# Performance work log

Hardware: AMD Instinct MI355X
Metric: run time of the kernel (lower is better)

Reference implementation:

```python
import jax, jax.numpy as jnp
import numpy as np

N = 4096
IN, HID, OUT = 512, 512, 512
EMB, MHID = 64, 128
GRID_SIZE, SPLINE_ORDER = 5, 3
D_B = GRID_SIZE + SPLINE_ORDER + 1      # 9
SPLINE_DIM = GRID_SIZE + SPLINE_ORDER   # 8


def make_grid():
    h = (1.0 - (-1.0)) / GRID_SIZE
    return jnp.arange(-SPLINE_ORDER, GRID_SIZE + SPLINE_ORDER + 1, dtype=jnp.float32) * h - 1.0


def b_splines(x, grid):
    # x: (N, in) -> (N, in, SPLINE_DIM); Cox-de Boor recursion, epsilon-stabilized
    xg = x[..., None]
    bases = ((xg >= grid[:-1]) & (xg < grid[1:])).astype(x.dtype)
    eps = 1e-08
    for k in range(1, SPLINE_ORDER + 1):
        dp = grid[k:-1] - grid[:-(k + 1)]
        dn = grid[k + 1:] - grid[1:-k]
        bases = (xg - grid[:-(k + 1)]) / (dp + eps) * bases[..., :-1] \
              + (grid[k + 1:] - xg) / (dn + eps) * bases[..., 1:]
    return bases


def _xavier(k, shape):
    fan_out, fan_in = shape
    std = (2.0 / (fan_in + fan_out)) ** 0.5
    return std * jax.random.normal(k, shape, jnp.float32)


def setup_inputs() -> dict:
    key = jax.random.key(0)
    ks = jax.random.split(key, 7)
    x = 2.0 * jax.random.uniform(ks[0], (N, IN), jnp.float32) - 1.0
    inp = {"x": x}
    dims = [(IN, HID), (HID, OUT)]
    for i, (fi, fo) in enumerate(dims):
        kk = jax.random.split(ks[i + 1], 3)
        inp[f"emb{i}"] = _xavier(kk[0], (fi * fo, EMB))   # layout: (out, in) flattened, out outer
        inp[f"w1_{i}"] = _xavier(kk[1], (MHID, EMB))
        inp[f"b1_{i}"] = jnp.zeros((MHID,), jnp.float32)
        inp[f"w2_{i}"] = _xavier(kk[2], (D_B, MHID))
        inp[f"b2_{i}"] = jnp.zeros((D_B,), jnp.float32)
    return inp


def _kan_layer(h, emb, w1, b1, w2, b2, in_f, out_f, grid):
    basis = b_splines(h, grid)                              # (N, in, SPLINE_DIM)
    w = (emb @ w1.T + b1) @ w2.T + b2                       # (out*in, D_B)
    w = w.reshape(out_f, in_f, D_B)
    w_spline = w[..., :SPLINE_DIM]                          # (out, in, SPLINE_DIM)
    w_base = w[..., SPLINE_DIM]                             # (out, in)  == weights[:, :, -1]
    out = jnp.einsum('nis,ois->no', basis, w_spline)
    out = out + jnp.einsum('ni,oi->no', jax.nn.silu(h), w_base)
    return out


def reference(x, emb0, w1_0, b1_0, w2_0, b2_0, emb1, w1_1, b1_1, w2_1, b2_1):
    grid = make_grid()
    h = _kan_layer(x, emb0, w1_0, b1_0, w2_0, b2_0, IN, HID, grid)
    h = _kan_layer(h, emb1, w1_1, b1_1, w2_1, b2_1, HID, OUT, grid)
    return h
```

## Files before the change

### kernel.cpp

```cpp
#include <hip/hip_runtime.h>
#include <cstdint>
#include <cstddef>

typedef unsigned short u16;
typedef unsigned int   u32;

typedef __bf16 bf16x8 __attribute__((ext_vector_type(8)));
typedef float  f32x4  __attribute__((ext_vector_type(4)));

#define NROWS 4096
#define INF   512
#define OUTF  512
#define EMB   64
#define MHID  128
#define DB    9
#define KDIM  (INF * DB)
#define MN    (NROWS * OUTF)

__device__ __forceinline__ u16 f2bf(float f) {
    union { float f; u32 ui; } v; v.f = f;
    u32 u = v.ui;
    u += 0x7fffu + ((u >> 16) & 1u);
    return (u16)(u >> 16);
}
__device__ __forceinline__ float gridv(int t) { return (float)(t - 3) * 0.4f - 1.0f; }

__global__ __launch_bounds__(256) void meff_kernel(
    const float* __restrict__ w1_0, const float* __restrict__ b1_0,
    const float* __restrict__ w2_0, const float* __restrict__ b2_0,
    const float* __restrict__ w1_1, const float* __restrict__ b1_1,
    const float* __restrict__ w2_1, const float* __restrict__ b2_1,
    float* __restrict__ Mc)
{
    int tid  = threadIdx.x;
    int lane = tid & 63;
    int wid  = blockIdx.x * 4 + (tid >> 6);
    if (wid >= 1170) return;
    int layer = wid / 585;
    int o     = wid % 585;
    const float* w1 = layer ? w1_1 : w1_0;
    const float* b1 = layer ? b1_1 : b1_0;
    const float* w2 = layer ? w2_1 : w2_0;
    const float* b2 = layer ? b2_1 : b2_0;

    float p;
    int d;
    if (o < 576) {
        int j = o / 9; d = o % 9;
        p = w1[lane * EMB + j]        * w2[d * MHID + lane]
          + w1[(lane + 64) * EMB + j] * w2[d * MHID + lane + 64];
    } else {
        d = o - 576;
        p = b1[lane] * w2[d * MHID + lane] + b1[lane + 64] * w2[d * MHID + lane + 64];
    }
#pragma unroll
    for (int off = 32; off >= 1; off >>= 1)
        p += __shfl_xor(p, off, 64);
    if (lane == 0) {
        if (o >= 576) p += b2[d];
        Mc[layer * 1024 + o] = p;
    }
}

__global__ __launch_bounds__(256) void genw_kernel(
    const float* __restrict__ emb0, const float* __restrict__ emb1,
    const float* __restrict__ Mc,
    u16* __restrict__ Bw0, u16* __restrict__ Bw1)
{
    __shared__ __align__(16) float tile[256 * 65];
    int layer = blockIdx.y;
    const float* emb = layer ? emb1 : emb0;
    u16* Bw = layer ? Bw1 : Bw0;
    const float* mc = Mc + layer * 1024;

    int tid = threadIdx.x;

    size_t rowbase = (size_t)blockIdx.x * 256;
    const float4* g4 = (const float4*)(emb + rowbase * EMB);
#pragma unroll
    for (int it = 0; it < 16; ++it) {
        int f = it * 256 + tid;
        float4 v = g4[f];
        int row = f >> 4, c4 = (f & 15) * 4;
        float* t = &tile[row * 65 + c4];
        t[0] = v.x; t[1] = v.y; t[2] = v.z; t[3] = v.w;
    }
    __syncthreads();

    float acc[9];
#pragma unroll
    for (int d = 0; d < 9; ++d) acc[d] = mc[576 + d];

    const float* myrow = &tile[tid * 65];
#pragma unroll
    for (int jj = 0; jj < 16; ++jj) {
        float v0 = myrow[jj * 4 + 0];
        float v1 = myrow[jj * 4 + 1];
        float v2 = myrow[jj * 4 + 2];
        float v3 = myrow[jj * 4 + 3];
#pragma unroll
        for (int d = 0; d < 9; ++d)
            acc[d] += v0 * mc[(jj * 4 + 0) * 9 + d]
                    + v1 * mc[(jj * 4 + 1) * 9 + d]
                    + v2 * mc[(jj * 4 + 2) * 9 + d]
                    + v3 * mc[(jj * 4 + 3) * 9 + d];
    }

    __syncthreads();
    u16* ob = (u16*)tile;
#pragma unroll
    for (int d = 0; d < 9; ++d) ob[tid * 9 + d] = f2bf(acc[d]);
    __syncthreads();

    const uint4* src = (const uint4*)ob;
    uint4* dst = (uint4*)(Bw + rowbase * 9);
    for (int s = tid; s < 288; s += 256) dst[s] = src[s];
}

__global__ __launch_bounds__(256) void phi_kernel(const float* __restrict__ xin,
                                                  const float* __restrict__ part,
                                                  int S,
                                                  u16* __restrict__ phi)
{
    __shared__ __align__(16) u16 lbuf[256 * 9];
    int tid = threadIdx.x;
    int idx = blockIdx.x * 256 + tid;

    float xv;
    if (part) {
        xv = 0.f;
        for (int z = 0; z < S; ++z) xv += part[(size_t)z * MN + idx];
    } else {
        xv = xin[idx];
    }

    float b[11];
#pragma unroll
    for (int t = 0; t < 11; ++t)
        b[t] = (xv >= gridv(t) && xv < gridv(t + 1)) ? 1.0f : 0.0f;
#pragma unroll
    for (int k = 1; k <= 3; ++k) {
#pragma unroll
        for (int t = 0; t + k < 11; ++t) {
            float rdp = 1.0f / ((gridv(t + k) - gridv(t)) + 1e-8f);
            float rdn = 1.0f / ((gridv(t + k + 1) - gridv(t + 1)) + 1e-8f);
            b[t] = (xv - gridv(t)) * rdp * b[t] + (gridv(t + k + 1) - xv) * rdn * b[t + 1];
        }
    }
    float sil = xv / (1.0f + expf(-xv));

#pragma unroll
    for (int d = 0; d < 8; ++d) lbuf[tid * 9 + d] = f2bf(b[d]);
    lbuf[tid * 9 + 8] = f2bf(sil);
    __syncthreads();

    const uint4* src = (const uint4*)lbuf;
    uint4* dst = (uint4*)(phi + (size_t)blockIdx.x * 256 * 9);
    for (int s = tid; s < 288; s += 256) dst[s] = src[s];
}

#define GLOAD16(gp, lp) __builtin_amdgcn_global_load_lds(                         \
    (const __attribute__((address_space(1))) u32*)(gp),                           \
    (__attribute__((address_space(3))) u32*)(lp), 16, 0, 0)

__global__ __launch_bounds__(256, 4) void gemm_kernel(const __bf16* __restrict__ A,
                                                      const __bf16* __restrict__ B,
                                                      float* __restrict__ Cpart,
                                                      int N, int K, int ksz)
{
    __shared__ __align__(16) __bf16 As[128 * 64];
    __shared__ __align__(16) __bf16 Bs[128 * 64];

    int tid  = threadIdx.x;
    int lane = tid & 63;
    int wv   = tid >> 6;
    int wm   = wv >> 1, wn = wv & 1;
    int brow = blockIdx.x * 128;
    int bcol = blockIdx.y * 128;
    int z    = blockIdx.z;
    int kbeg = z * ksz, kend = kbeg + ksz;

    f32x4 acc[4][4];
#pragma unroll
    for (int r = 0; r < 4; ++r)
#pragma unroll
        for (int c = 0; c < 4; ++c)
#pragma unroll
            for (int g = 0; g < 4; ++g) acc[r][c][g] = 0.0f;

    int quad = lane >> 4;
    int l16  = lane & 15;

    for (int k0 = kbeg; k0 < kend; k0 += 64) {
#pragma unroll
        for (int q = 0; q < 4; ++q) {
            int chunk = q * 256 + wv * 64 + lane;
            int row   = chunk >> 3;
            int slot  = chunk & 7;
            int col   = ((slot ^ (row & 7)) << 3);
            const __bf16* ga = A + (size_t)(brow + row) * K + (k0 + col);
            const __bf16* gb = B + (size_t)(bcol + row) * K + (k0 + col);
            GLOAD16(ga, &As[(q * 256 + wv * 64) * 8]);
            GLOAD16(gb, &Bs[(q * 256 + wv * 64) * 8]);
        }
        __syncthreads();

#pragma unroll
        for (int ks = 0; ks < 2; ++ks) {
            bf16x8 af[4], bfr[4];
#pragma unroll
            for (int r = 0; r < 4; ++r) {
                int arow = wm * 64 + r * 16 + l16;
                af[r] = *(const bf16x8*)&As[arow * 64 + (((ks * 4 + quad) ^ (arow & 7)) << 3)];
                int brw = wn * 64 + r * 16 + l16;
                bfr[r] = *(const bf16x8*)&Bs[brw * 64 + (((ks * 4 + quad) ^ (brw & 7)) << 3)];
            }
#pragma unroll
            for (int r = 0; r < 4; ++r)
#pragma unroll
                for (int c = 0; c < 4; ++c)
                    acc[r][c] = __builtin_amdgcn_mfma_f32_16x16x32_bf16(af[r], bfr[c], acc[r][c], 0, 0, 0);
        }
        __syncthreads();
    }

    float* Cz = Cpart + (size_t)z * MN;
#pragma unroll
    for (int r = 0; r < 4; ++r)
#pragma unroll
        for (int c = 0; c < 4; ++c)
#pragma unroll
            for (int g = 0; g < 4; ++g) {
                int grow = brow + wm * 64 + r * 16 + quad * 4 + g;
                int gcol = bcol + wn * 64 + c * 16 + l16;
                Cz[(size_t)grow * N + gcol] = acc[r][c][g];
            }
}

__global__ __launch_bounds__(256) void reduce_kernel(const float* __restrict__ part,
                                                     int S, float* __restrict__ out)
{
    int i = blockIdx.x * 256 + threadIdx.x;
    const float4* p4 = (const float4*)part;
    float4 s = p4[i];
    for (int z = 1; z < S; ++z) {
        float4 v = p4[(size_t)z * (MN / 4) + i];
        s.x += v.x; s.y += v.y; s.z += v.z; s.w += v.w;
    }
    ((float4*)out)[i] = s;
}

extern "C" void kernel_launch(void* const* d_in, const int* in_sizes, int n_in,
                              void* d_out, int out_size, void* d_ws, size_t ws_size,
                              hipStream_t stream)
{
    const float* x    = (const float*)d_in[0];
    const float* emb0 = (const float*)d_in[1];
    const float* w1_0 = (const float*)d_in[2];
    const float* b1_0 = (const float*)d_in[3];
    const float* w2_0 = (const float*)d_in[4];
    const float* b2_0 = (const float*)d_in[5];
    const float* emb1 = (const float*)d_in[6];
    const float* w1_1 = (const float*)d_in[7];
    const float* b1_1 = (const float*)d_in[8];
    const float* w2_1 = (const float*)d_in[9];
    const float* b2_1 = (const float*)d_in[10];

    char* ws = (char*)d_ws;
    const size_t PHI_OFF  = 0;
    const size_t BW0_OFF  = 37748736;
    const size_t BW1_OFF  = BW0_OFF + 4718592;
    const size_t MC_OFF   = BW1_OFF + 4718592;
    const size_t PART_OFF = MC_OFF + 8192;

    int S = 1;
    const size_t SLAB = 8388608ull;
    if      (ws_size >= PART_OFF + 4 * SLAB) S = 4;
    else if (ws_size >= PART_OFF + 2 * SLAB) S = 2;
    int ksz = KDIM / S;

    u16*   phi  = (u16*)(ws + PHI_OFF);
    u16*   Bw0  = (u16*)(ws + BW0_OFF);
    u16*   Bw1  = (u16*)(ws + BW1_OFF);
    float* Mc   = (float*)(ws + MC_OFF);
    float* part = (float*)(ws + PART_OFF);

    meff_kernel<<<293, 256, 0, stream>>>(w1_0, b1_0, w2_0, b2_0,
                                         w1_1, b1_1, w2_1, b2_1, Mc);
    genw_kernel<<<dim3(1024, 2), 256, 0, stream>>>(emb0, emb1, Mc, Bw0, Bw1);

    phi_kernel<<<8192, 256, 0, stream>>>(x, nullptr, 0, phi);
    gemm_kernel<<<dim3(32, 4, S), 256, 0, stream>>>((const __bf16*)phi, (const __bf16*)Bw0,
                                                    part, OUTF, KDIM, ksz);
    phi_kernel<<<8192, 256, 0, stream>>>(nullptr, part, S, phi);
    gemm_kernel<<<dim3(32, 4, S), 256, 0, stream>>>((const __bf16*)phi, (const __bf16*)Bw1,
                                                    part, OUTF, KDIM, ksz);
    reduce_kernel<<<2048, 256, 0, stream>>>(part, S, (float*)d_out);
}
```

Baseline: 270.8 us.

## Split genw rows across two threads with swizzled float4 LDS tile

Each genw block now handles 128 embedding rows instead of 256. Two threads share one row, each covering half of the 64 embedding columns, and their partial sums are combined through shared memory. The LDS tile is stored as XOR-swizzled float4 instead of padded scalars, which allows vector LDS reads without bank conflicts. LDS per block drops from about 66KB to about 35KB, which raises occupancy and doubles the grid, at the cost of an extra reduction step and one more barrier.

```diff
diff --git a/kernel.cpp b/kernel.cpp
--- a/kernel.cpp
+++ b/kernel.cpp
@@ -67,54 +67,61 @@
     const float* __restrict__ Mc,
     u16* __restrict__ Bw0, u16* __restrict__ Bw1)
 {
-    __shared__ __align__(16) float tile[256 * 65];
+    __shared__ __align__(16) float4 tile[128 * 16];
+    __shared__ __align__(16) float  pbuf[128 * 9];
+    __shared__ __align__(16) u16    ob[128 * 9];
     int layer = blockIdx.y;
     const float* emb = layer ? emb1 : emb0;
     u16* Bw = layer ? Bw1 : Bw0;
     const float* mc = Mc + layer * 1024;
 
     int tid = threadIdx.x;
-
-    size_t rowbase = (size_t)blockIdx.x * 256;
+    size_t rowbase = (size_t)blockIdx.x * 128;
+
     const float4* g4 = (const float4*)(emb + rowbase * EMB);
 #pragma unroll
-    for (int it = 0; it < 16; ++it) {
-        int f = it * 256 + tid;
+    for (int q = 0; q < 8; ++q) {
+        int f = q * 256 + tid;
         float4 v = g4[f];
-        int row = f >> 4, c4 = (f & 15) * 4;
-        float* t = &tile[row * 65 + c4];
-        t[0] = v.x; t[1] = v.y; t[2] = v.z; t[3] = v.w;
+        int row = f >> 4, c4 = f & 15;
+        tile[row * 16 + (c4 ^ (row & 15))] = v;
     }
     __syncthreads();
 
+    int r  = tid & 127;
+    int hi = tid >> 7;
+    int cb = hi * 8;
+    const float* mcp = mc + __builtin_amdgcn_readfirstlane(hi) * 32 * 9;
+
     float acc[9];
 #pragma unroll
-    for (int d = 0; d < 9; ++d) acc[d] = mc[576 + d];
-
-    const float* myrow = &tile[tid * 65];
-#pragma unroll
-    for (int jj = 0; jj < 16; ++jj) {
-        float v0 = myrow[jj * 4 + 0];
-        float v1 = myrow[jj * 4 + 1];
-        float v2 = myrow[jj * 4 + 2];
-        float v3 = myrow[jj * 4 + 3];
+    for (int d = 0; d < 9; ++d) acc[d] = hi ? 0.0f : mc[576 + d];
+
+#pragma unroll
+    for (int jj = 0; jj < 8; ++jj) {
+        float4 v = tile[r * 16 + ((cb + jj) ^ (r & 15))];
 #pragma unroll
         for (int d = 0; d < 9; ++d)
-            acc[d] += v0 * mc[(jj * 4 + 0) * 9 + d]
-                    + v1 * mc[(jj * 4 + 1) * 9 + d]
-                    + v2 * mc[(jj * 4 + 2) * 9 + d]
-                    + v3 * mc[(jj * 4 + 3) * 9 + d];
-    }
-
+            acc[d] += v.x * mcp[(jj * 4 + 0) * 9 + d]
+                    + v.y * mcp[(jj * 4 + 1) * 9 + d]
+                    + v.z * mcp[(jj * 4 + 2) * 9 + d]
+                    + v.w * mcp[(jj * 4 + 3) * 9 + d];
+    }
+
+    if (hi) {
+#pragma unroll
+        for (int d = 0; d < 9; ++d) pbuf[r * 9 + d] = acc[d];
+    }
     __syncthreads();
-    u16* ob = (u16*)tile;
-#pragma unroll
-    for (int d = 0; d < 9; ++d) ob[tid * 9 + d] = f2bf(acc[d]);
+    if (!hi) {
+#pragma unroll
+        for (int d = 0; d < 9; ++d) ob[r * 9 + d] = f2bf(acc[d] + pbuf[r * 9 + d]);
+    }
     __syncthreads();
 
     const uint4* src = (const uint4*)ob;
     uint4* dst = (uint4*)(Bw + rowbase * 9);
-    for (int s = tid; s < 288; s += 256) dst[s] = src[s];
+    if (tid < 144) dst[tid] = src[tid];
 }
 
 __global__ __launch_bounds__(256) void phi_kernel(const float* __restrict__ xin,
@@ -287,7 +294,7 @@
 
     meff_kernel<<<293, 256, 0, stream>>>(w1_0, b1_0, w2_0, b2_0,
                                          w1_1, b1_1, w2_1, b2_1, Mc);
-    genw_kernel<<<dim3(1024, 2), 256, 0, stream>>>(emb0, emb1, Mc, Bw0, Bw1);
+    genw_kernel<<<dim3(2048, 2), 256, 0, stream>>>(emb0, emb1, Mc, Bw0, Bw1);
 
     phi_kernel<<<8192, 256, 0, stream>>>(x, nullptr, 0, phi);
     gemm_kernel<<<dim3(32, 4, S), 256, 0, stream>>>((const __bf16*)phi, (const __bf16*)Bw0,
```

Result: faster. 260.9 us (-3.7%).
